# Kernel tuning notes

Hardware: AMD Instinct MI355X
Metric: run time of the kernel (lower is better)

Reference implementation:

```python
import jax, jax.numpy as jnp
import numpy as np
from jax import lax

B, N, D = 64, 499, 256          # batch, nodes(=seq_len), emb_size
NUM_P, NUM_Q, NUM_C = 10000, 2000, 10


def _seg_softmax(e, dst, n):
    # e: [E,H] edge scores, segment softmax over destination node
    m = jax.ops.segment_max(e, dst, num_segments=n)
    ex = jnp.exp(e - m[dst])
    s = jax.ops.segment_sum(ex, dst, num_segments=n)
    return ex / s[dst]


def gat_conv(x, src, dst, W, a_src, a_dst, b, concat):
    # x: [B,n,Fin], W: [Fin,H*Fo], a_src/a_dst: [H,Fo], b: [H*Fo] or [Fo]
    Bn, n, _ = x.shape
    H, Fo = a_src.shape
    h = (x @ W).reshape(Bn, n, H, Fo)
    es = jnp.einsum('bnhf,hf->bnh', h, a_src)
    ed = jnp.einsum('bnhf,hf->bnh', h, a_dst)
    e = jax.nn.leaky_relu(es[:, src] + ed[:, dst], 0.2)   # [B,E,H]
    alpha = jax.vmap(lambda eb: _seg_softmax(eb, dst, n))(e)
    msg = alpha[..., None] * h[:, src]                    # [B,E,H,Fo]
    out = jax.vmap(lambda mb: jax.ops.segment_sum(mb, dst, num_segments=n))(msg)
    out = out.reshape(Bn, n, H * Fo) if concat else out.mean(axis=2)
    return out + b


def lstm(xs, W_ih, W_hh, b_ih, b_hh):
    # xs: [B,S,I]; torch gate order i,f,g,o
    Bn = xs.shape[0]
    Hd = W_hh.shape[1]

    def step(carry, xt):
        h, c = carry
        g = xt @ W_ih.T + b_ih + h @ W_hh.T + b_hh
        i, f, gg, o = jnp.split(g, 4, axis=-1)
        c = jax.nn.sigmoid(f) * c + jax.nn.sigmoid(i) * jnp.tanh(gg)
        h = jax.nn.sigmoid(o) * jnp.tanh(c)
        return (h, c), h

    init = (jnp.zeros((Bn, Hd), xs.dtype), jnp.zeros((Bn, Hd), xs.dtype))
    _, hs = lax.scan(step, init, xs.transpose(1, 0, 2))
    return hs.transpose(1, 0, 2)


def _edges():
    # genr_edge_index(true_length-1=498): chain over nodes 0..497, then
    # PyG GATConv removes self-loops and adds them back for all 499 nodes.
    L = N - 1
    src, dst = [], []
    for i in range(L):
        for j in (i - 1, i + 1):
            if 0 <= j < L:
                src.append(i)
                dst.append(j)
    src += list(range(N))
    dst += list(range(N))
    return np.array(src, np.int32), np.array(dst, np.int32)


def setup_inputs() -> dict:
    key = jax.random.key(0)
    ks = jax.random.split(key, 30)
    f32 = jnp.float32

    def nrm(k, shape, s=0.05):
        return jax.random.normal(k, shape, dtype=f32) * s

    src, dst = _edges()
    inp = {
        'true_length': jnp.full((B,), N, dtype=jnp.int32),
        'p': jax.random.randint(ks[0], (B, N), 0, NUM_P + 1, dtype=jnp.int32),
        'q': jax.random.randint(ks[1], (B, N), 0, NUM_Q + 1, dtype=jnp.int32),
        'r': jax.random.randint(ks[2], (B, N), 0, 2, dtype=jnp.int32),
        'aff': jax.random.randint(ks[3], (B, N), 0, NUM_C + 1, dtype=jnp.int32),
        'q_next': jax.random.randint(ks[4], (B, N), 0, NUM_Q + 1, dtype=jnp.int32),
        'p_next': jax.random.randint(ks[5], (B, N), 0, NUM_P + 1, dtype=jnp.int32),
        'src': jnp.asarray(src),
        'dst': jnp.asarray(dst),
        'emb_p': nrm(ks[6], (NUM_P + 1, D), 1.0),
        'emb_q': nrm(ks[7], (NUM_Q + 1, D), 1.0),
        'emb_r': nrm(ks[8], (2, D), 1.0),
        'emb_aff': nrm(ks[9], (NUM_C + 1, D), 1.0),
        'W_affcat': nrm(ks[10], (2 * D, D)),
        'b_affcat': nrm(ks[11], (D,)),
        'W_g1': nrm(ks[12], (D, 8 * 128)),
        'a_src1': nrm(ks[13], (8, 128)),
        'a_dst1': nrm(ks[14], (8, 128)),
        'b_g1': nrm(ks[15], (8 * 128,)),
        'W_g2': nrm(ks[16], (8 * 128, D)),
        'a_src2': nrm(ks[17], (1, D)),
        'a_dst2': nrm(ks[18], (1, D)),
        'b_g2': nrm(ks[19], (D,)),
        'W_ih': nrm(ks[20], (4 * D, 4 * D)),
        'W_hh': nrm(ks[21], (4 * D, D)),
        'b_ih': nrm(ks[22], (4 * D,)),
        'b_hh': nrm(ks[23], (4 * D,)),
        'W_out': nrm(ks[24], (3 * D, 1)),
        'b_out': nrm(ks[25], (1,)),
    }
    return inp


def reference(true_length, p, q, r, aff, q_next, p_next, src, dst,
              emb_p, emb_q, emb_r, emb_aff, W_affcat, b_affcat,
              W_g1, a_src1, a_dst1, b_g1, W_g2, a_src2, a_dst2, b_g2,
              W_ih, W_hh, b_ih, b_hh, W_out, b_out):
    # eval mode: all dropouts are identity
    p_emb = emb_p[p]            # [B,N,D]
    q_emb = emb_q[q]
    r_emb = emb_r[r]
    qn_emb = emb_q[q_next]
    pn_emb = emb_p[p_next]
    aff_emb = emb_aff[aff]

    x = jnp.concatenate([p_emb, aff_emb], axis=-1) @ W_affcat + b_affcat
    x = jax.nn.elu(gat_conv(x, src, dst, W_g1, a_src1, a_dst1, b_g1, True))
    x = gat_conv(x, src, dst, W_g2, a_src2, a_dst2, b_g2, False)   # [B,N,D]

    seq = jnp.concatenate([p_emb, q_emb, r_emb, x], axis=-1)       # [B,N,4D]
    h = lstm(seq, W_ih, W_hh, b_ih, b_hh)                          # [B,N,D]
    y = jnp.concatenate([h, qn_emb, pn_emb], axis=-1) @ W_out + b_out
    return jax.nn.sigmoid(y)
```

## Files before the change

### kernel.cpp

```cpp
#include <hip/hip_runtime.h>
#include <hip/hip_bf16.h>

typedef unsigned int u32;
typedef unsigned short u16;

#define MTOT 31936
#define NN 499
#define BB 64

__device__ __forceinline__ float lo16(u32 u){ return __uint_as_float(u << 16); }
__device__ __forceinline__ float hi16(u32 u){ return __uint_as_float(u & 0xffff0000u); }
__device__ __forceinline__ float bf2f(u16 u){ return __uint_as_float(((u32)u) << 16); }
__device__ __forceinline__ u16 f2bf(float f){
  u32 x = __float_as_uint(f);
  u32 r = (x + 0x7fffu + ((x >> 16) & 1u)) >> 16;
  return (u16)r;
}
__device__ __forceinline__ float sigf(float x){ return 1.f / (1.f + __expf(-x)); }
__device__ __forceinline__ float tanh_(float x){ return 2.f * sigf(2.f * x) - 1.f; }
__device__ __forceinline__ float wred(float v){
  #pragma unroll
  for (int off = 32; off; off >>= 1) v += __shfl_down(v, off, 64);
  return v;
}

typedef __attribute__((ext_vector_type(2))) __bf16 bf16x2;

#if __has_builtin(__builtin_amdgcn_cvt_pk_bf16_f32)
__device__ __forceinline__ u32 pk2bf(float a, float b){
  union { bf16x2 v; u32 u; } r;
  r.v = __builtin_amdgcn_cvt_pk_bf16_f32(a, b);
  return r.u;
}
#else
__device__ __forceinline__ u32 pk2bf(float a, float b){
  return (u32)f2bf(a) | ((u32)f2bf(b) << 16);
}
#endif

typedef __attribute__((ext_vector_type(8))) short bfrag8;
typedef __attribute__((ext_vector_type(4))) float f4_t;
union FragU { uint4 u; bfrag8 s; };

__device__ __forceinline__ f4_t mfma16(FragU a, FragU b, f4_t c){
  return __builtin_amdgcn_mfma_f32_16x16x32_bf16(a.s, b.s, c, 0, 0, 0);
}

template <typename AL>
__device__ __forceinline__ void gemm_core2(int K32, const uint4* __restrict__ Bpack,
                                           int ntBase, f4_t (&acc)[4][2], AL aload){
  __shared__ __align__(16) uint4 As[2][256];
  const int tid = threadIdx.x;
  const int lane = tid & 63;
  const uint4* Bp0 = Bpack + ((size_t)ntBase * K32) * 64 + lane;
  const uint4* Bp1 = Bp0 + (size_t)K32 * 64;
  int buf = 0;
  for (int kt = 0; kt < K32; kt++){
    FragU b0, b1;
    b0.u = Bp0[kt * 64];
    b1.u = Bp1[kt * 64];
    As[buf][tid] = aload(kt);
    __syncthreads();
    FragU a0, a1, a2, a3;
    a0.u = As[buf][lane];
    a1.u = As[buf][64 + lane];
    a2.u = As[buf][128 + lane];
    a3.u = As[buf][192 + lane];
    acc[0][0] = mfma16(a0, b0, acc[0][0]); acc[0][1] = mfma16(a0, b1, acc[0][1]);
    acc[1][0] = mfma16(a1, b0, acc[1][0]); acc[1][1] = mfma16(a1, b1, acc[1][1]);
    acc[2][0] = mfma16(a2, b0, acc[2][0]); acc[2][1] = mfma16(a2, b1, acc[2][1]);
    acc[3][0] = mfma16(a3, b0, acc[3][0]); acc[3][1] = mfma16(a3, b1, acc[3][1]);
    buf ^= 1;
  }
}

__global__ __launch_bounds__(256) void k_packB(const float* __restrict__ W, u16* __restrict__ out,
                                               int K, int N, int trans){
  int c = blockIdx.x * 256 + threadIdx.x;
  int K32 = K >> 5;
  int total = (N >> 4) * K32 * 64;
  if (c >= total) return;
  int l = c & 63;
  int rem = c >> 6;
  int kt = rem % K32, nt = rem / K32;
  int n = nt * 16 + (l & 15);
  int kb = kt * 32 + (l >> 4) * 8;
  u32 ov[4];
  #pragma unroll
  for (int j2 = 0; j2 < 4; j2++){
    int k = kb + j2 * 2;
    float f0 = trans ? W[(size_t)n * K + k]     : W[(size_t)k * N + n];
    float f1 = trans ? W[(size_t)n * K + k + 1] : W[(size_t)(k + 1) * N + n];
    ov[j2] = pk2bf(f0, f1);
  }
  uint4 o; o.x = ov[0]; o.y = ov[1]; o.z = ov[2]; o.w = ov[3];
  *(uint4*)(out + (size_t)c * 8) = o;
}

__global__ void k_csr(const int* __restrict__ src, const int* __restrict__ dst, int E,
                      int* __restrict__ deg, int* __restrict__ insrc){
  int tid = threadIdx.x;
  for (int i = tid; i < NN; i += 256) deg[i] = 0;
  for (int i = tid; i < NN * 4; i += 256) insrc[i] = 0;
  __syncthreads();
  for (int e = tid; e < E; e += 256){
    int d = dst[e];
    int slot = atomicAdd(&deg[d], 1);
    if (slot < 4) insrc[d * 4 + slot] = src[e];
  }
}

__global__ __launch_bounds__(256) void k_affcat_m(
    const float* __restrict__ emb_p, const float* __restrict__ emb_aff,
    const int* __restrict__ p, const int* __restrict__ aff,
    const uint4* __restrict__ Bpack, const float* __restrict__ bias, float* __restrict__ C){
  const int tid = threadIdx.x;
  const int mBase = blockIdx.x * 64, nBase = blockIdx.y * 128;
  const int ls = tid & 63;
  const int gm = mBase + (tid >> 6) * 16 + (ls & 15);
  const int kqoff = (ls >> 4) * 8;
  const float* rp = emb_p + (size_t)p[gm] * 256 + kqoff;
  const float* ra = emb_aff + (size_t)aff[gm] * 256 + kqoff;
  f4_t acc[4][2] = {};
  gemm_core2(16, Bpack, blockIdx.y * 8 + ((tid >> 6) << 1), acc, [&](int kt) -> uint4 {
    int kb = kt * 32;
    const float* s = (kb < 256) ? (rp + kb) : (ra + kb - 256);
    float4 v0 = *(const float4*)s;
    float4 v1 = *(const float4*)(s + 4);
    uint4 o; o.x = pk2bf(v0.x, v0.y); o.y = pk2bf(v0.z, v0.w);
    o.z = pk2bf(v1.x, v1.y); o.w = pk2bf(v1.z, v1.w);
    return o;
  });
  const int wave = tid >> 6, lane = tid & 63;
  const int rb = (lane >> 4) << 2;
  const int cbase = nBase + wave * 32 + (lane & 15);
  float b0 = bias[cbase], b1 = bias[cbase + 16];
  #pragma unroll
  for (int i = 0; i < 4; i++)
    #pragma unroll
    for (int r = 0; r < 4; r++){
      int row = mBase + i * 16 + rb + r;
      C[(size_t)row * 256 + cbase]      = acc[i][0][r] + b0;
      C[(size_t)row * 256 + cbase + 16] = acc[i][1][r] + b1;
    }
}

__global__ __launch_bounds__(256) void k_h1_m(const float* __restrict__ A,
                                              const uint4* __restrict__ Bpack,
                                              u16* __restrict__ Cb){
  const int tid = threadIdx.x;
  const int mBase = blockIdx.x * 64, nBase = blockIdx.y * 128;
  const int ls = tid & 63;
  const int gm = mBase + (tid >> 6) * 16 + (ls & 15);
  const float* ra = A + (size_t)gm * 256 + (ls >> 4) * 8;
  f4_t acc[4][2] = {};
  gemm_core2(8, Bpack, blockIdx.y * 8 + ((tid >> 6) << 1), acc, [&](int kt) -> uint4 {
    const float* s = ra + kt * 32;
    float4 v0 = *(const float4*)s;
    float4 v1 = *(const float4*)(s + 4);
    uint4 o; o.x = pk2bf(v0.x, v0.y); o.y = pk2bf(v0.z, v0.w);
    o.z = pk2bf(v1.x, v1.y); o.w = pk2bf(v1.z, v1.w);
    return o;
  });
  const int wave = tid >> 6, lane = tid & 63;
  const int rb = (lane >> 4) << 2;
  const int cbase = nBase + wave * 32 + (lane & 15);
  #pragma unroll
  for (int i = 0; i < 4; i++)
    #pragma unroll
    for (int r = 0; r < 4; r++){
      int row = mBase + i * 16 + rb + r;
      Cb[(size_t)row * 1024 + cbase]      = f2bf(acc[i][0][r]);
      Cb[(size_t)row * 1024 + cbase + 16] = f2bf(acc[i][1][r]);
    }
}

__global__ __launch_bounds__(256) void k_h2_m(const u16* __restrict__ A,
                                              const uint4* __restrict__ Bpack,
                                              float* __restrict__ C){
  const int tid = threadIdx.x;
  const int mBase = blockIdx.x * 64, nBase = blockIdx.y * 128;
  const int ls = tid & 63;
  const int gm = mBase + (tid >> 6) * 16 + (ls & 15);
  const u16* ra = A + (size_t)gm * 1024 + (ls >> 4) * 8;
  f4_t acc[4][2] = {};
  gemm_core2(32, Bpack, blockIdx.y * 8 + ((tid >> 6) << 1), acc, [&](int kt) -> uint4 {
    return *(const uint4*)(ra + kt * 32);
  });
  const int wave = tid >> 6, lane = tid & 63;
  const int rb = (lane >> 4) << 2;
  const int cbase = nBase + wave * 32 + (lane & 15);
  #pragma unroll
  for (int i = 0; i < 4; i++)
    #pragma unroll
    for (int r = 0; r < 4; r++){
      int row = mBase + i * 16 + rb + r;
      C[(size_t)row * 256 + cbase]      = acc[i][0][r];
      C[(size_t)row * 256 + cbase + 16] = acc[i][1][r];
    }
}

__global__ __launch_bounds__(256) void k_gates_m(
    const float* __restrict__ emb_p, const float* __restrict__ emb_q, const float* __restrict__ emb_r,
    const int* __restrict__ p, const int* __restrict__ q, const int* __restrict__ r,
    const float* __restrict__ x2, const uint4* __restrict__ Bpack,
    const float* __restrict__ bih, const float* __restrict__ bhh, u16* __restrict__ Cb){
  const int tid = threadIdx.x;
  const int mBase = blockIdx.x * 64, nBase = blockIdx.y * 128;
  const int ls = tid & 63;
  const int gm = mBase + (tid >> 6) * 16 + (ls & 15);
  const int kqoff = (ls >> 4) * 8;
  const float* s0 = emb_p + (size_t)p[gm] * 256 + kqoff;
  const float* s1 = emb_q + (size_t)q[gm] * 256 + kqoff;
  const float* s2 = emb_r + (size_t)r[gm] * 256 + kqoff;
  const float* s3 = x2 + (size_t)gm * 256 + kqoff;
  f4_t acc[4][2] = {};
  gemm_core2(32, Bpack, blockIdx.y * 8 + ((tid >> 6) << 1), acc, [&](int kt) -> uint4 {
    int kb = kt * 32;
    int seg = kb >> 8, ko = kb & 255;
    const float* s = (seg == 0) ? s0 : ((seg == 1) ? s1 : ((seg == 2) ? s2 : s3));
    float4 v0 = *(const float4*)(s + ko);
    float4 v1 = *(const float4*)(s + ko + 4);
    uint4 o; o.x = pk2bf(v0.x, v0.y); o.y = pk2bf(v0.z, v0.w);
    o.z = pk2bf(v1.x, v1.y); o.w = pk2bf(v1.z, v1.w);
    return o;
  });
  const int wave = tid >> 6, lane = tid & 63;
  const int rb = (lane >> 4) << 2;
  const int cbase = nBase + wave * 32 + (lane & 15);
  float b0 = bih[cbase] + bhh[cbase];
  float b1 = bih[cbase + 16] + bhh[cbase + 16];
  #pragma unroll
  for (int i = 0; i < 4; i++)
    #pragma unroll
    for (int r2 = 0; r2 < 4; r2++){
      int row = mBase + i * 16 + rb + r2;
      Cb[(size_t)row * 1024 + cbase]      = f2bf(acc[i][0][r2] + b0);
      Cb[(size_t)row * 1024 + cbase + 16] = f2bf(acc[i][1][r2] + b1);
    }
}

__global__ __launch_bounds__(256) void k_repack2(const u16* __restrict__ gates,
                                                 u16* __restrict__ G2){
  __shared__ __align__(16) u16 staged[1024];
  const int tid = threadIdx.x;
  const size_t m = blockIdx.x;
  const u32* row32 = (const u32*)(gates + m * 1024);
  ((u32*)staged)[tid]       = row32[tid];
  ((u32*)staged)[tid + 256] = row32[tid + 256];
  __syncthreads();
  if (tid < 128){
    const int w = tid >> 4, uc = tid & 15;
    u32 vw[4];
    #pragma unroll
    for (int j = 0; j < 4; j++){
      const int P = j >> 1, glo = (j & 1) * 2;
      const u16 lo = staged[glo * 256 + w * 32 + P * 16 + uc];
      const u16 hi = staged[(glo + 1) * 256 + w * 32 + P * 16 + uc];
      vw[j] = (u32)lo | ((u32)hi << 16);
    }
    uint4 o; o.x = vw[0]; o.y = vw[1]; o.z = vw[2]; o.w = vw[3];
    *(uint4*)(G2 + (m * 128 + (size_t)tid) * 8) = o;
  }
}

__global__ __launch_bounds__(256) void k_esed(
    const u16* __restrict__ hb, const float* __restrict__ hf,
    const float* __restrict__ asrc, const float* __restrict__ adst,
    float* __restrict__ es, float* __restrict__ ed, int Hm1, int Fo){
  int w = blockIdx.x * 4 + (threadIdx.x >> 6);
  int lane = threadIdx.x & 63;
  int h = w & Hm1;
  size_t base = (size_t)w * Fo;
  float s = 0.f, d = 0.f;
  for (int f = lane; f < Fo; f += 64){
    float hv = hb ? bf2f(hb[base + f]) : hf[base + f];
    s += hv * asrc[h * Fo + f];
    d += hv * adst[h * Fo + f];
  }
  s = wred(s); d = wred(d);
  if (!lane){ es[w] = s; ed[w] = d; }
}

__global__ __launch_bounds__(256) void k_gatagg(
    const u16* __restrict__ hb, const float* __restrict__ hf,
    const float* __restrict__ es, const float* __restrict__ ed,
    const int* __restrict__ deg, const int* __restrict__ insrc,
    const float* __restrict__ bias, u16* __restrict__ outb, float* __restrict__ outf,
    int H, int foShift, int HFo, int do_elu){
  int m = blockIdx.x;
  int b = m / NN;
  int n = m - b * NN;
  int dg = deg[n];
  int s0 = insrc[n * 4 + 0];
  int s1 = insrc[n * 4 + 1];
  int s2 = insrc[n * 4 + 2];
  int rowBase = b * NN;
  for (int c = threadIdx.x; c < HFo; c += 256){
    int h = c >> foShift;
    float edv = ed[(size_t)m * H + h];
    float sc0 = es[(size_t)(rowBase + s0) * H + h] + edv;
    sc0 = (sc0 >= 0.f) ? sc0 : 0.2f * sc0;
    float sc1 = 0.f, sc2 = 0.f, mx = sc0;
    if (dg > 1){ sc1 = es[(size_t)(rowBase + s1) * H + h] + edv; sc1 = (sc1 >= 0.f) ? sc1 : 0.2f * sc1; mx = fmaxf(mx, sc1); }
    if (dg > 2){ sc2 = es[(size_t)(rowBase + s2) * H + h] + edv; sc2 = (sc2 >= 0.f) ? sc2 : 0.2f * sc2; mx = fmaxf(mx, sc2); }
    float e0 = __expf(sc0 - mx), e1 = 0.f, e2 = 0.f;
    if (dg > 1) e1 = __expf(sc1 - mx);
    if (dg > 2) e2 = __expf(sc2 - mx);
    float inv = 1.f / (e0 + e1 + e2);
    size_t c0 = (size_t)(rowBase + s0) * HFo + c;
    float acc = e0 * (hb ? bf2f(hb[c0]) : hf[c0]);
    if (dg > 1){ size_t c1 = (size_t)(rowBase + s1) * HFo + c; acc += e1 * (hb ? bf2f(hb[c1]) : hf[c1]); }
    if (dg > 2){ size_t c2 = (size_t)(rowBase + s2) * HFo + c; acc += e2 * (hb ? bf2f(hb[c2]) : hf[c2]); }
    acc *= inv;
    float o = acc + bias[c];
    if (do_elu) o = (o > 0.f) ? o : (__expf(o) - 1.f);
    if (outb) outb[(size_t)m * HFo + c] = f2bf(o);
    else      outf[(size_t)m * HFo + c] = o;
  }
}

#define WREG 32
#define WLDS 17
__global__ __launch_bounds__(512)
__attribute__((amdgpu_waves_per_eu(2, 2)))
void k_lstm(const u16* __restrict__ g2,
            const uint4* __restrict__ bph,
            float* __restrict__ h_all){
  __shared__ __align__(16) uint4 wlds[8][WLDS][64];
  __shared__ __align__(16) u16 hsh[2][256];
  const int b = blockIdx.x, tid = threadIdx.x;
  const int w = tid >> 6, lane = tid & 63;
  const int uc = lane & 15, oct = lane >> 4;
  if (tid < 64) ((u32*)hsh[1])[tid & 63] = 0u;
  if (tid < 128) ((u32*)hsh[1])[tid] = 0u;

  uint4 wreg[WREG];
  #pragma unroll
  for (int kc = 0; kc < 8; kc++)
    #pragma unroll
    for (int g = 0; g < 3; g++)
      wreg[kc * 3 + g] = bph[(size_t)(((g * 16 + w * 2) * 8 + kc) * 64) + lane];
  wreg[24] = bph[(size_t)(((48 + w * 2) * 8) * 64) + lane];
  #pragma unroll
  for (int kc = 1; kc < 8; kc++)
    wreg[24 + kc] = bph[(size_t)(((32 + w * 2 + 1) * 8 + kc) * 64) + lane];
  #pragma unroll
  for (int kc = 0; kc < 8; kc++){
    wlds[w][kc][lane]     = bph[(size_t)(((w * 2 + 1) * 8 + kc) * 64) + lane];
    wlds[w][8 + kc][lane] = bph[(size_t)(((16 + w * 2 + 1) * 8 + kc) * 64) + lane];
  }
  wlds[w][16][lane] = bph[(size_t)(((32 + w * 2 + 1) * 8) * 64) + lane];

  const uint4* sp = bph + (size_t)(((48 + w * 2) * 8) * 64) + lane;

  const uint4* g0p = (const uint4*)g2 + (size_t)b * NN * 128 + w * 16 + uc;
  uint4 G0q = *g0p;
  g0p += 128;

  const size_t hofs0 = ((size_t)b * NN) * 256 + (size_t)w * 32 + uc;
  float cst[2] = {0.f, 0.f};

  uint4 wstr[6];
  #pragma unroll
  for (int s = 0; s < 6; s++) wstr[s] = sp[(s + 1) * 64];
  __syncthreads();

  #pragma unroll 1
  for (int n = 0; n < NN; n++){
    const char* hrd = (const char*)hsh[(n + 1) & 1];
    char* hwr = (char*)hsh[n & 1];
    float hv2[2];
    #pragma unroll
    for (int P = 0; P < 2; P++){
      f4_t acc[4] = {};
      #pragma unroll
      for (int kc = 0; kc < 8; kc++){
        const int ph = P * 8 + kc;
        FragU a;
        a.u = *(const uint4*)(hrd + (u32)(kc * 64 + oct * 16));
        #pragma unroll
        for (int g = 0; g < 4; g++){
          FragU bb;
          if (P == 0){
            if (g < 3)            bb.u = wreg[kc * 3 + g];
            else if (kc == 0)     bb.u = wreg[24];
            else                  bb.u = wstr[(ph - 1) % 6];
          } else {
            if (g == 0)           bb.u = wlds[w][kc][lane];
            else if (g == 1)      bb.u = wlds[w][8 + kc][lane];
            else if (g == 2)      bb.u = (kc == 0) ? wlds[w][16][lane] : wreg[24 + kc];
            else                  bb.u = wstr[(ph - 1) % 6];
          }
          acc[g] = mfma16(a, bb, acc[g]);
        }
        if (ph >= 1 && ph <= 9)
          wstr[(ph + 5) % 6] = sp[(ph + 6) * 64];
      }
      if (P == 1){
        #pragma unroll
        for (int s = 0; s < 6; s++) wstr[s] = sp[(s + 1) * 64];
      }
      float gv[4];
      #pragma unroll
      for (int g = 0; g < 4; g++){
        const int wi = P * 2 + (g >> 1);
        const u32 uw = (wi == 0) ? G0q.x : (wi == 1) ? G0q.y : (wi == 2) ? G0q.z : G0q.w;
        gv[g] = acc[g][0] + ((g & 1) ? hi16(uw) : lo16(uw));
      }
      const float cv = sigf(gv[1]) * cst[P] + sigf(gv[0]) * tanh_(gv[2]);
      cst[P] = cv;
      hv2[P] = sigf(gv[3]) * tanh_(cv);
    }
    if (oct == 0){
      #pragma unroll
      for (int P = 0; P < 2; P++){
        const int u = w * 32 + P * 16 + uc;
        *(u16*)(hwr + u * 2) = f2bf(hv2[P]);
        h_all[hofs0 + (size_t)n * 256 + P * 16] = hv2[P];
      }
    }
    if (n + 1 < NN){
      G0q = *g0p;
      g0p += 128;
    }
    asm volatile("s_waitcnt lgkmcnt(0)" ::: "memory");
    __builtin_amdgcn_s_barrier();
    __builtin_amdgcn_sched_barrier(0);
  }
}

__global__ __launch_bounds__(256) void k_out(const float* __restrict__ h_all,
    const float* __restrict__ emb_q, const float* __restrict__ emb_p,
    const int* __restrict__ qn, const int* __restrict__ pn,
    const float* __restrict__ Wo, const float* __restrict__ bo, float* __restrict__ y){
  int m = blockIdx.x * 4 + (threadIdx.x >> 6);
  int lane = threadIdx.x & 63;
  const float* hr = h_all + (size_t)m * 256;
  const float* rq = emb_q + (size_t)qn[m] * 256;
  const float* rp = emb_p + (size_t)pn[m] * 256;
  float acc = 0.f;
  #pragma unroll
  for (int f = 0; f < 256; f += 64){
    int d = f + lane;
    acc += hr[d] * Wo[d];
    acc += rq[d] * Wo[256 + d];
    acc += rp[d] * Wo[512 + d];
  }
  acc = wred(acc);
  if (!lane) y[m] = sigf(acc + bo[0]);
}

extern "C" void kernel_launch(void* const* d_in, const int* in_sizes, int n_in,
                              void* d_out, int out_size, void* d_ws, size_t ws_size,
                              hipStream_t stream){
  (void)n_in; (void)out_size; (void)ws_size;
  const int* p    = (const int*)d_in[1];
  const int* q    = (const int*)d_in[2];
  const int* r    = (const int*)d_in[3];
  const int* aff  = (const int*)d_in[4];
  const int* qn   = (const int*)d_in[5];
  const int* pn   = (const int*)d_in[6];
  const int* src  = (const int*)d_in[7];
  const int* dst  = (const int*)d_in[8];
  const float* emb_p  = (const float*)d_in[9];
  const float* emb_q  = (const float*)d_in[10];
  const float* emb_r  = (const float*)d_in[11];
  const float* emb_aff= (const float*)d_in[12];
  const float* W_aff  = (const float*)d_in[13];
  const float* b_aff  = (const float*)d_in[14];
  const float* W_g1   = (const float*)d_in[15];
  const float* a_s1   = (const float*)d_in[16];
  const float* a_d1   = (const float*)d_in[17];
  const float* b_g1   = (const float*)d_in[18];
  const float* W_g2   = (const float*)d_in[19];
  const float* a_s2   = (const float*)d_in[20];
  const float* a_d2   = (const float*)d_in[21];
  const float* b_g2   = (const float*)d_in[22];
  const float* W_ih   = (const float*)d_in[23];
  const float* W_hh   = (const float*)d_in[24];
  const float* b_ih   = (const float*)d_in[25];
  const float* b_hh   = (const float*)d_in[26];
  const float* W_out  = (const float*)d_in[27];
  const float* b_out  = (const float*)d_in[28];
  const int E = in_sizes[7];

  char* ws = (char*)d_ws;
  size_t off = 0;
  auto alloc = [&](size_t bytes){ size_t ret = off; off += (bytes + 255) & ~(size_t)255; return ret; };
  size_t o_bigA = alloc((size_t)MTOT * 1024 * 2);
  size_t o_bigB = alloc((size_t)MTOT * 1024 * 2);
  size_t o_buf3 = alloc((size_t)MTOT * 256 * 4);
  size_t o_es1 = alloc((size_t)MTOT * 8 * 4);
  size_t o_ed1 = alloc((size_t)MTOT * 8 * 4);
  size_t o_es2 = alloc((size_t)MTOT * 4);
  size_t o_ed2 = alloc((size_t)MTOT * 4);
  size_t o_whh = alloc((size_t)32768 * 16);
  size_t o_deg = alloc(512 * 4);
  size_t o_ins = alloc((size_t)NN * 4 * 4);
  size_t o_bpih  = alloc((size_t)131072 * 16);
  size_t o_bpg1  = alloc((size_t)32768 * 16);
  size_t o_bpg2  = alloc((size_t)32768 * 16);
  size_t o_bpaff = alloc((size_t)16384 * 16);

  u16*   h1    = (u16*)(ws + o_bigA);
  u16*   gates = (u16*)(ws + o_bigA);
  u16*   g1out = (u16*)(ws + o_bigB);
  float* x2    = (float*)(ws + o_bigB);
  u16*   G2    = (u16*)(ws + o_bigB);
  float* x0    = (float*)(ws + o_buf3);
  float* h2    = (float*)(ws + o_buf3);
  float* h_all = (float*)(ws + o_buf3);
  float* es1   = (float*)(ws + o_es1);
  float* ed1   = (float*)(ws + o_ed1);
  float* es2   = (float*)(ws + o_es2);
  float* ed2   = (float*)(ws + o_ed2);
  u16*   bphh  = (u16*)(ws + o_whh);
  int*   degp  = (int*)(ws + o_deg);
  int*   insp  = (int*)(ws + o_ins);
  u16*   bpih  = (u16*)(ws + o_bpih);
  u16*   bpg1  = (u16*)(ws + o_bpg1);
  u16*   bpg2  = (u16*)(ws + o_bpg2);
  u16*   bpaff = (u16*)(ws + o_bpaff);

  k_csr<<<1, 256, 0, stream>>>(src, dst, E, degp, insp);
  k_packB<<<128, 256, 0, stream>>>(W_hh, bphh, 256, 1024, 1);
  k_packB<<<512, 256, 0, stream>>>(W_ih, bpih, 1024, 1024, 1);
  k_packB<<<128, 256, 0, stream>>>(W_g1, bpg1, 256, 1024, 0);
  k_packB<<<128, 256, 0, stream>>>(W_g2, bpg2, 1024, 256, 0);
  k_packB<<<64, 256, 0, stream>>>(W_aff, bpaff, 512, 256, 0);

  k_affcat_m<<<dim3(NN, 2), 256, 0, stream>>>(emb_p, emb_aff, p, aff,
                                              (const uint4*)bpaff, b_aff, x0);
  k_h1_m<<<dim3(NN, 8), 256, 0, stream>>>(x0, (const uint4*)bpg1, h1);
  k_esed<<<(MTOT * 8) / 4, 256, 0, stream>>>(h1, nullptr, a_s1, a_d1, es1, ed1, 7, 128);
  k_gatagg<<<MTOT, 256, 0, stream>>>(h1, nullptr, es1, ed1, degp, insp, b_g1,
                                     g1out, nullptr, 8, 7, 1024, 1);
  k_h2_m<<<dim3(NN, 2), 256, 0, stream>>>(g1out, (const uint4*)bpg2, h2);
  k_esed<<<MTOT / 4, 256, 0, stream>>>(nullptr, h2, a_s2, a_d2, es2, ed2, 0, 256);
  k_gatagg<<<MTOT, 256, 0, stream>>>(nullptr, h2, es2, ed2, degp, insp, b_g2,
                                     nullptr, x2, 1, 8, 256, 0);
  k_gates_m<<<dim3(NN, 8), 256, 0, stream>>>(emb_p, emb_q, emb_r, p, q, r, x2,
                                             (const uint4*)bpih, b_ih, b_hh, gates);
  k_repack2<<<MTOT, 256, 0, stream>>>(gates, G2);
  k_lstm<<<BB, 512, 0, stream>>>(G2, (const uint4*)bphh, h_all);
  k_out<<<MTOT / 4, 256, 0, stream>>>(h_all, emb_q, emb_p, qn, pn, W_out, b_out, (float*)d_out);
}
```

Before: 1.529 ms.

## Pre-convert embeddings to bf16 and stream GEMM A tiles via global_load_lds

Embedding tables are converted to bf16 once per call, and the intermediate activations x0 and x2 are stored as bf16 instead of fp32. This halves the bytes read by the GEMM A-loaders and lets them issue direct global-to-LDS loads without passing through registers. The LSTM step also issues all 16 MFMA phases into 8 accumulators before the gate math, which gives more instruction-level parallelism. In exchange it adds pack kernels that read the full embedding tables each call, and x2 is now rounded to bf16. The gatagg call reuses its bf16 output slot for x2, so it depends on that kernel's flag semantics.

```diff
diff --git a/kernel.cpp b/kernel.cpp
--- a/kernel.cpp
+++ b/kernel.cpp
@@ -38,6 +38,9 @@
 }
 #endif
 
+typedef __attribute__((address_space(1))) void AS1void;
+typedef __attribute__((address_space(3))) void AS3void;
+
 typedef __attribute__((ext_vector_type(8))) short bfrag8;
 typedef __attribute__((ext_vector_type(4))) float f4_t;
 union FragU { uint4 u; bfrag8 s; };
@@ -46,12 +49,12 @@
   return __builtin_amdgcn_mfma_f32_16x16x32_bf16(a.s, b.s, c, 0, 0, 0);
 }
 
-template <typename AL>
-__device__ __forceinline__ void gemm_core2(int K32, const uint4* __restrict__ Bpack,
-                                           int ntBase, f4_t (&acc)[4][2], AL aload){
+template <typename AP>
+__device__ __forceinline__ void gemm_core3(int K32, const uint4* __restrict__ Bpack,
+                                           int ntBase, f4_t (&acc)[4][2], AP aaddr){
   __shared__ __align__(16) uint4 As[2][256];
   const int tid = threadIdx.x;
-  const int lane = tid & 63;
+  const int wave = tid >> 6, lane = tid & 63;
   const uint4* Bp0 = Bpack + ((size_t)ntBase * K32) * 64 + lane;
   const uint4* Bp1 = Bp0 + (size_t)K32 * 64;
   int buf = 0;
@@ -59,7 +62,8 @@
     FragU b0, b1;
     b0.u = Bp0[kt * 64];
     b1.u = Bp1[kt * 64];
-    As[buf][tid] = aload(kt);
+    __builtin_amdgcn_global_load_lds((AS1void*)aaddr(kt),
+                                     (AS3void*)&As[buf][wave * 64], 16, 0, 0);
     __syncthreads();
     FragU a0, a1, a2, a3;
     a0.u = As[buf][lane];
@@ -72,6 +76,15 @@
     acc[3][0] = mfma16(a3, b0, acc[3][0]); acc[3][1] = mfma16(a3, b1, acc[3][1]);
     buf ^= 1;
   }
+}
+
+__global__ __launch_bounds__(256) void k_packE(const float* __restrict__ in,
+                                               u16* __restrict__ out, int n4){
+  int i = blockIdx.x * 256 + threadIdx.x;
+  if (i >= n4) return;
+  float4 v = ((const float4*)in)[i];
+  uint2 o; o.x = pk2bf(v.x, v.y); o.y = pk2bf(v.z, v.w);
+  ((uint2*)out)[i] = o;
 }
 
 __global__ __launch_bounds__(256) void k_packB(const float* __restrict__ W, u16* __restrict__ out,
@@ -111,25 +124,20 @@
 }
 
 __global__ __launch_bounds__(256) void k_affcat_m(
-    const float* __restrict__ emb_p, const float* __restrict__ emb_aff,
+    const u16* __restrict__ emb_pb, const u16* __restrict__ emb_ab,
     const int* __restrict__ p, const int* __restrict__ aff,
-    const uint4* __restrict__ Bpack, const float* __restrict__ bias, float* __restrict__ C){
+    const uint4* __restrict__ Bpack, const float* __restrict__ bias, u16* __restrict__ Cb){
   const int tid = threadIdx.x;
   const int mBase = blockIdx.x * 64, nBase = blockIdx.y * 128;
   const int ls = tid & 63;
   const int gm = mBase + (tid >> 6) * 16 + (ls & 15);
   const int kqoff = (ls >> 4) * 8;
-  const float* rp = emb_p + (size_t)p[gm] * 256 + kqoff;
-  const float* ra = emb_aff + (size_t)aff[gm] * 256 + kqoff;
+  const u16* rp = emb_pb + (size_t)p[gm] * 256 + kqoff;
+  const u16* ra = emb_ab + (size_t)aff[gm] * 256 + kqoff;
   f4_t acc[4][2] = {};
-  gemm_core2(16, Bpack, blockIdx.y * 8 + ((tid >> 6) << 1), acc, [&](int kt) -> uint4 {
+  gemm_core3(16, Bpack, blockIdx.y * 8 + ((tid >> 6) << 1), acc, [&](int kt) -> const void* {
     int kb = kt * 32;
-    const float* s = (kb < 256) ? (rp + kb) : (ra + kb - 256);
-    float4 v0 = *(const float4*)s;
-    float4 v1 = *(const float4*)(s + 4);
-    uint4 o; o.x = pk2bf(v0.x, v0.y); o.y = pk2bf(v0.z, v0.w);
-    o.z = pk2bf(v1.x, v1.y); o.w = pk2bf(v1.z, v1.w);
-    return o;
+    return (kb < 256) ? (const void*)(rp + kb) : (const void*)(ra + kb - 256);
   });
   const int wave = tid >> 6, lane = tid & 63;
   const int rb = (lane >> 4) << 2;
@@ -140,27 +148,22 @@
     #pragma unroll
     for (int r = 0; r < 4; r++){
       int row = mBase + i * 16 + rb + r;
-      C[(size_t)row * 256 + cbase]      = acc[i][0][r] + b0;
-      C[(size_t)row * 256 + cbase + 16] = acc[i][1][r] + b1;
-    }
-}
-
-__global__ __launch_bounds__(256) void k_h1_m(const float* __restrict__ A,
+      Cb[(size_t)row * 256 + cbase]      = f2bf(acc[i][0][r] + b0);
+      Cb[(size_t)row * 256 + cbase + 16] = f2bf(acc[i][1][r] + b1);
+    }
+}
+
+__global__ __launch_bounds__(256) void k_h1_m(const u16* __restrict__ A,
                                               const uint4* __restrict__ Bpack,
                                               u16* __restrict__ Cb){
   const int tid = threadIdx.x;
   const int mBase = blockIdx.x * 64, nBase = blockIdx.y * 128;
   const int ls = tid & 63;
   const int gm = mBase + (tid >> 6) * 16 + (ls & 15);
-  const float* ra = A + (size_t)gm * 256 + (ls >> 4) * 8;
+  const u16* ra = A + (size_t)gm * 256 + (ls >> 4) * 8;
   f4_t acc[4][2] = {};
-  gemm_core2(8, Bpack, blockIdx.y * 8 + ((tid >> 6) << 1), acc, [&](int kt) -> uint4 {
-    const float* s = ra + kt * 32;
-    float4 v0 = *(const float4*)s;
-    float4 v1 = *(const float4*)(s + 4);
-    uint4 o; o.x = pk2bf(v0.x, v0.y); o.y = pk2bf(v0.z, v0.w);
-    o.z = pk2bf(v1.x, v1.y); o.w = pk2bf(v1.z, v1.w);
-    return o;
+  gemm_core3(8, Bpack, blockIdx.y * 8 + ((tid >> 6) << 1), acc, [&](int kt) -> const void* {
+    return (const void*)(ra + kt * 32);
   });
   const int wave = tid >> 6, lane = tid & 63;
   const int rb = (lane >> 4) << 2;
@@ -184,8 +187,8 @@
   const int gm = mBase + (tid >> 6) * 16 + (ls & 15);
   const u16* ra = A + (size_t)gm * 1024 + (ls >> 4) * 8;
   f4_t acc[4][2] = {};
-  gemm_core2(32, Bpack, blockIdx.y * 8 + ((tid >> 6) << 1), acc, [&](int kt) -> uint4 {
-    return *(const uint4*)(ra + kt * 32);
+  gemm_core3(32, Bpack, blockIdx.y * 8 + ((tid >> 6) << 1), acc, [&](int kt) -> const void* {
+    return (const void*)(ra + kt * 32);
   });
   const int wave = tid >> 6, lane = tid & 63;
   const int rb = (lane >> 4) << 2;
@@ -201,29 +204,25 @@
 }
 
 __global__ __launch_bounds__(256) void k_gates_m(
-    const float* __restrict__ emb_p, const float* __restrict__ emb_q, const float* __restrict__ emb_r,
+    const u16* __restrict__ emb_pb, const u16* __restrict__ emb_qb, const u16* __restrict__ emb_rb,
     const int* __restrict__ p, const int* __restrict__ q, const int* __restrict__ r,
-    const float* __restrict__ x2, const uint4* __restrict__ Bpack,
+    const u16* __restrict__ x2b, const uint4* __restrict__ Bpack,
     const float* __restrict__ bih, const float* __restrict__ bhh, u16* __restrict__ Cb){
   const int tid = threadIdx.x;
   const int mBase = blockIdx.x * 64, nBase = blockIdx.y * 128;
   const int ls = tid & 63;
   const int gm = mBase + (tid >> 6) * 16 + (ls & 15);
   const int kqoff = (ls >> 4) * 8;
-  const float* s0 = emb_p + (size_t)p[gm] * 256 + kqoff;
-  const float* s1 = emb_q + (size_t)q[gm] * 256 + kqoff;
-  const float* s2 = emb_r + (size_t)r[gm] * 256 + kqoff;
-  const float* s3 = x2 + (size_t)gm * 256 + kqoff;
+  const u16* s0 = emb_pb + (size_t)p[gm] * 256 + kqoff;
+  const u16* s1 = emb_qb + (size_t)q[gm] * 256 + kqoff;
+  const u16* s2 = emb_rb + (size_t)r[gm] * 256 + kqoff;
+  const u16* s3 = x2b + (size_t)gm * 256 + kqoff;
   f4_t acc[4][2] = {};
-  gemm_core2(32, Bpack, blockIdx.y * 8 + ((tid >> 6) << 1), acc, [&](int kt) -> uint4 {
+  gemm_core3(32, Bpack, blockIdx.y * 8 + ((tid >> 6) << 1), acc, [&](int kt) -> const void* {
     int kb = kt * 32;
     int seg = kb >> 8, ko = kb & 255;
-    const float* s = (seg == 0) ? s0 : ((seg == 1) ? s1 : ((seg == 2) ? s2 : s3));
-    float4 v0 = *(const float4*)(s + ko);
-    float4 v1 = *(const float4*)(s + ko + 4);
-    uint4 o; o.x = pk2bf(v0.x, v0.y); o.y = pk2bf(v0.z, v0.w);
-    o.z = pk2bf(v1.x, v1.y); o.w = pk2bf(v1.z, v1.w);
-    return o;
+    const u16* s = (seg == 0) ? s0 : ((seg == 1) ? s1 : ((seg == 2) ? s2 : s3));
+    return (const void*)(s + ko);
   });
   const int wave = tid >> 6, lane = tid & 63;
   const int rb = (lane >> 4) << 2;
@@ -332,7 +331,6 @@
   const int b = blockIdx.x, tid = threadIdx.x;
   const int w = tid >> 6, lane = tid & 63;
   const int uc = lane & 15, oct = lane >> 4;
-  if (tid < 64) ((u32*)hsh[1])[tid & 63] = 0u;
   if (tid < 128) ((u32*)hsh[1])[tid] = 0u;
 
   uint4 wreg[WREG];
@@ -370,43 +368,41 @@
   for (int n = 0; n < NN; n++){
     const char* hrd = (const char*)hsh[(n + 1) & 1];
     char* hwr = (char*)hsh[n & 1];
+    f4_t acc[8] = {};
+    #pragma unroll
+    for (int ph = 0; ph < 16; ph++){
+      const int P = ph >> 3, kc = ph & 7;
+      FragU a;
+      a.u = *(const uint4*)(hrd + (u32)(kc * 64 + oct * 16));
+      #pragma unroll
+      for (int g = 0; g < 4; g++){
+        FragU bb;
+        if (P == 0){
+          if (g < 3)            bb.u = wreg[kc * 3 + g];
+          else if (kc == 0)     bb.u = wreg[24];
+          else                  bb.u = wstr[(ph - 1) % 6];
+        } else {
+          if (g == 0)           bb.u = wlds[w][kc][lane];
+          else if (g == 1)      bb.u = wlds[w][8 + kc][lane];
+          else if (g == 2)      bb.u = (kc == 0) ? wlds[w][16][lane] : wreg[24 + kc];
+          else                  bb.u = wstr[(ph - 1) % 6];
+        }
+        acc[P * 4 + g] = mfma16(a, bb, acc[P * 4 + g]);
+      }
+      if (ph >= 1 && ph <= 9)
+        wstr[(ph + 5) % 6] = sp[(ph + 6) * 64];
+    }
+    #pragma unroll
+    for (int s = 0; s < 6; s++) wstr[s] = sp[(s + 1) * 64];
     float hv2[2];
     #pragma unroll
     for (int P = 0; P < 2; P++){
-      f4_t acc[4] = {};
-      #pragma unroll
-      for (int kc = 0; kc < 8; kc++){
-        const int ph = P * 8 + kc;
-        FragU a;
-        a.u = *(const uint4*)(hrd + (u32)(kc * 64 + oct * 16));
-        #pragma unroll
-        for (int g = 0; g < 4; g++){
-          FragU bb;
-          if (P == 0){
-            if (g < 3)            bb.u = wreg[kc * 3 + g];
-            else if (kc == 0)     bb.u = wreg[24];
-            else                  bb.u = wstr[(ph - 1) % 6];
-          } else {
-            if (g == 0)           bb.u = wlds[w][kc][lane];
-            else if (g == 1)      bb.u = wlds[w][8 + kc][lane];
-            else if (g == 2)      bb.u = (kc == 0) ? wlds[w][16][lane] : wreg[24 + kc];
-            else                  bb.u = wstr[(ph - 1) % 6];
-          }
-          acc[g] = mfma16(a, bb, acc[g]);
-        }
-        if (ph >= 1 && ph <= 9)
-          wstr[(ph + 5) % 6] = sp[(ph + 6) * 64];
-      }
-      if (P == 1){
-        #pragma unroll
-        for (int s = 0; s < 6; s++) wstr[s] = sp[(s + 1) * 64];
-      }
       float gv[4];
       #pragma unroll
       for (int g = 0; g < 4; g++){
         const int wi = P * 2 + (g >> 1);
         const u32 uw = (wi == 0) ? G0q.x : (wi == 1) ? G0q.y : (wi == 2) ? G0q.z : G0q.w;
-        gv[g] = acc[g][0] + ((g & 1) ? hi16(uw) : lo16(uw));
+        gv[g] = acc[P * 4 + g][0] + ((g & 1) ? hi16(uw) : lo16(uw));
       }
       const float cv = sigf(gv[1]) * cst[P] + sigf(gv[0]) * tanh_(gv[2]);
       cst[P] = cv;
@@ -502,13 +498,17 @@
   size_t o_bpg1  = alloc((size_t)32768 * 16);
   size_t o_bpg2  = alloc((size_t)32768 * 16);
   size_t o_bpaff = alloc((size_t)16384 * 16);
+  size_t o_ebp = alloc((size_t)10001 * 256 * 2);
+  size_t o_ebq = alloc((size_t)2001 * 256 * 2);
+  size_t o_ebr = alloc((size_t)2 * 256 * 2);
+  size_t o_eba = alloc((size_t)11 * 256 * 2);
 
   u16*   h1    = (u16*)(ws + o_bigA);
   u16*   gates = (u16*)(ws + o_bigA);
   u16*   g1out = (u16*)(ws + o_bigB);
-  float* x2    = (float*)(ws + o_bigB);
+  u16*   x2b   = (u16*)(ws + o_bigB);
   u16*   G2    = (u16*)(ws + o_bigB);
-  float* x0    = (float*)(ws + o_buf3);
+  u16*   x0b   = (u16*)(ws + o_buf3);
   float* h2    = (float*)(ws + o_buf3);
   float* h_all = (float*)(ws + o_buf3);
   float* es1   = (float*)(ws + o_es1);
@@ -522,6 +522,10 @@
   u16*   bpg1  = (u16*)(ws + o_bpg1);
   u16*   bpg2  = (u16*)(ws + o_bpg2);
   u16*   bpaff = (u16*)(ws + o_bpaff);
+  u16*   ebp   = (u16*)(ws + o_ebp);
+  u16*   ebq   = (u16*)(ws + o_ebq);
+  u16*   ebr   = (u16*)(ws + o_ebr);
+  u16*   eba   = (u16*)(ws + o_eba);
 
   k_csr<<<1, 256, 0, stream>>>(src, dst, E, degp, insp);
   k_packB<<<128, 256, 0, stream>>>(W_hh, bphh, 256, 1024, 1);
@@ -529,18 +533,22 @@
   k_packB<<<128, 256, 0, stream>>>(W_g1, bpg1, 256, 1024, 0);
   k_packB<<<128, 256, 0, stream>>>(W_g2, bpg2, 1024, 256, 0);
   k_packB<<<64, 256, 0, stream>>>(W_aff, bpaff, 512, 256, 0);
-
-  k_affcat_m<<<dim3(NN, 2), 256, 0, stream>>>(emb_p, emb_aff, p, aff,
-                                              (const uint4*)bpaff, b_aff, x0);
-  k_h1_m<<<dim3(NN, 8), 256, 0, stream>>>(x0, (const uint4*)bpg1, h1);
+  k_packE<<<2501, 256, 0, stream>>>(emb_p, ebp, 10001 * 64);
+  k_packE<<<501, 256, 0, stream>>>(emb_q, ebq, 2001 * 64);
+  k_packE<<<1, 256, 0, stream>>>(emb_r, ebr, 2 * 64);
+  k_packE<<<3, 256, 0, stream>>>(emb_aff, eba, 11 * 64);
+
+  k_affcat_m<<<dim3(NN, 2), 256, 0, stream>>>(ebp, eba, p, aff,
+                                              (const uint4*)bpaff, b_aff, x0b);
+  k_h1_m<<<dim3(NN, 8), 256, 0, stream>>>(x0b, (const uint4*)bpg1, h1);
   k_esed<<<(MTOT * 8) / 4, 256, 0, stream>>>(h1, nullptr, a_s1, a_d1, es1, ed1, 7, 128);
   k_gatagg<<<MTOT, 256, 0, stream>>>(h1, nullptr, es1, ed1, degp, insp, b_g1,
                                      g1out, nullptr, 8, 7, 1024, 1);
   k_h2_m<<<dim3(NN, 2), 256, 0, stream>>>(g1out, (const uint4*)bpg2, h2);
   k_esed<<<MTOT / 4, 256, 0, stream>>>(nullptr, h2, a_s2, a_d2, es2, ed2, 0, 256);
   k_gatagg<<<MTOT, 256, 0, stream>>>(nullptr, h2, es2, ed2, degp, insp, b_g2,
-                                     nullptr, x2, 1, 8, 256, 0);
-  k_gates_m<<<dim3(NN, 8), 256, 0, stream>>>(emb_p, emb_q, emb_r, p, q, r, x2,
+                                     x2b, nullptr, 1, 8, 256, 0);
+  k_gates_m<<<dim3(NN, 8), 256, 0, stream>>>(ebp, ebq, ebr, p, q, r, x2b,
                                              (const uint4*)bpih, b_ih, b_hh, gates);
   k_repack2<<<MTOT, 256, 0, stream>>>(gates, G2);
   k_lstm<<<BB, 512, 0, stream>>>(G2, (const uint4*)bphh, h_all);
```

After: 1.485 ms, median of 3. 2.9% less time.
